# Kernel tuning notes

Measured on AMD Instinct MI355X. Metric: run time of the kernel, lower is better.

Reference implementation:

```python
import jax, jax.numpy as jnp
import numpy as np

CCA_W, INTRA_W, AUX_W, OS_W, RFS_W = 0.1, 0.05, 1.0, 1.0, 1.0


def cox_loss(risk, events, times):
    # Efron-tied Cox partial likelihood, vectorized over tie groups.
    order = jnp.argsort(-times)  # descending time
    r = risk[order]
    e = events[order]
    t = times[order]
    B = r.shape[0]
    max_r = jnp.max(r)
    exp_r = jnp.exp(r - max_r)
    cum = jnp.cumsum(exp_r)  # risk-set sums (descending time => cumsum)
    # contiguous tie groups (times sorted, ties adjacent)
    new_grp = jnp.concatenate([jnp.zeros(1, jnp.int32), (t[1:] != t[:-1]).astype(jnp.int32)])
    gid = jnp.cumsum(new_grp)
    rss = jax.ops.segment_max(cum, gid, num_segments=B)[gid]          # cum_exp_risk at last idx of group
    tes = jax.ops.segment_sum(exp_r * e, gid, num_segments=B)[gid]     # tied exp-risk sum
    d = jax.ops.segment_sum(e, gid, num_segments=B)[gid]               # tie count (events)
    # rank l of each event within its tie group (0..d-1)
    c = jnp.cumsum(e)
    start = jax.ops.segment_min(jnp.arange(B), gid, num_segments=B)[gid]
    before = c[start] - e[start]
    l = c - 1.0 - before
    d_safe = jnp.where(d > 0, d, 1.0)
    denom = rss - (l / d_safe) * tes
    contrib = e * (r - jnp.log(denom + 1e-12) - max_r)
    n_events = jnp.sum(e)
    return -jnp.sum(contrib) / (n_events + 1e-12)


def distance_correlation_loss(za, zb):
    def dist(x):
        xx = jnp.sum(x * x, axis=1, keepdims=True)
        d2 = xx + xx.T - 2.0 * (x @ x.T)
        return jnp.sqrt(jnp.maximum(d2, 1e-8))
    def dc(D):
        return D - D.mean(axis=1, keepdims=True) - D.mean(axis=0, keepdims=True) + D.mean()
    A = dc(dist(za))
    Bm = dc(dist(zb))
    dcov = jnp.mean(A * Bm)
    va = jnp.mean(A * A)
    vb = jnp.mean(Bm * Bm)
    return 1.0 - dcov / jnp.sqrt(jnp.maximum(va * vb, 1e-8))


def setup_inputs() -> dict:
    key = jax.random.key(0)
    ks = jax.random.split(key, 10)
    B, D = 8192, 256
    return {
        'risk_os': jax.random.normal(ks[0], (B,), jnp.float32),
        'risk_rfs': jax.random.normal(ks[1], (B,), jnp.float32),
        'z_ct': jax.random.normal(ks[2], (B, D), jnp.float32),
        'z_wsi': jax.random.normal(ks[3], (B, D), jnp.float32),
        'intra_wsi': jax.random.uniform(ks[4], (), jnp.float32),
        'intra_ct': jax.random.uniform(ks[5], (), jnp.float32),
        'evt_os': jax.random.randint(ks[6], (B,), 0, 2, jnp.int32),
        'tm_os': jax.random.randint(ks[7], (B,), 0, 1000, jnp.int32),
        'evt_rfs': jax.random.randint(ks[8], (B,), 0, 2, jnp.int32),
        'tm_rfs': jax.random.randint(ks[9], (B,), 0, 1000, jnp.int32),
    }


def reference(risk_os, risk_rfs, z_ct, z_wsi, intra_wsi, intra_ct,
              evt_os, tm_os, evt_rfs, tm_rfs):
    l_os = cox_loss(risk_os, evt_os.astype(jnp.float32), tm_os.astype(jnp.float32))
    l_rfs = cox_loss(risk_rfs, evt_rfs.astype(jnp.float32), tm_rfs.astype(jnp.float32))
    l_cca = distance_correlation_loss(z_ct, z_wsi)
    l_intra = intra_wsi + intra_ct
    total = OS_W * l_os + RFS_W * l_rfs + AUX_W * (CCA_W * l_cca + INTRA_W * l_intra)
    return total
```

## Files before the change

### kernel.cpp

```cpp
#include <hip/hip_runtime.h>
#include <hip/hip_bf16.h>
#include <math.h>

typedef __attribute__((ext_vector_type(4))) float f32x4;
typedef __attribute__((ext_vector_type(4))) int int4v;

#define NBINS 1000

__device__ __forceinline__ void gl16(const void* g, void* l) {
  __builtin_amdgcn_global_load_lds(
      (const __attribute__((address_space(1))) unsigned int*)g,
      (__attribute__((address_space(3))) unsigned int*)l, 16, 0, 0);
}

__device__ __forceinline__ float fp8mag(unsigned b) {
  const int e = (b >> 3) & 15;
  const int m = b & 7;
  return e ? ldexpf((float)(8 + m), e - 10) : ldexpf((float)m, -9);
}

__global__ __launch_bounds__(256)
void prep_kernel(const float* __restrict__ za, const float* __restrict__ zb,
                 float* __restrict__ na, float* __restrict__ nb,
                 unsigned char* __restrict__ zpa, unsigned char* __restrict__ zpb,
                 int B, int D)
{
  const int row = blockIdx.x * 4 + (threadIdx.x >> 6);
  const int lane = threadIdx.x & 63;
  const float* src; float* dst; unsigned char* bd; int r;
  if (row < B) { src = za; dst = na; bd = zpa; r = row; }
  else         { src = zb; dst = nb; bd = zpb; r = row - B; }
  const int pt = r >> 7;
  const int rr = r & 127;
  const int sw = (rr >> 1) & 3;
  const size_t tbase = (size_t)pt * 128 * D;
  float s = 0.f;
  for (int c = lane * 4; c < D; c += 256) {
    const f32x4 v = *(const f32x4*)&src[(size_t)r * D + c];
    unsigned u = (unsigned)__builtin_amdgcn_cvt_pk_fp8_f32(v[0], v[1], 0, false);
    u = (unsigned)__builtin_amdgcn_cvt_pk_fp8_f32(v[2], v[3], (int)u, true);
    const int sc = c >> 6;
    const int half = (c >> 5) & 1;
    const int kg = (c >> 3) & 3;
    const int rem = c & 7;
    const int slot = kg ^ sw;
    *(unsigned*)&bd[tbase + sc * 8192 + rr * 64 + slot * 16 + half * 8 + rem] = u;
    const float x0 = fp8mag(u & 255), x1 = fp8mag((u >> 8) & 255);
    const float x2 = fp8mag((u >> 16) & 255), x3 = fp8mag(u >> 24);
    s += x0 * x0 + x1 * x1 + x2 * x2 + x3 * x3;
  }
#pragma unroll
  for (int off = 32; off; off >>= 1) s += __shfl_xor(s, off);
  if (lane == 0) dst[r] = s;
}

__global__ __launch_bounds__(256, 2)
void dcor_kernel(const unsigned char* __restrict__ zpa,
                 const unsigned char* __restrict__ zpb,
                 const float* __restrict__ na, const float* __restrict__ nb,
                 float* __restrict__ Ra, float* __restrict__ Rb,
                 double* __restrict__ scalPart,
                 const float* __restrict__ r0, const int* __restrict__ e0, const int* __restrict__ t0,
                 const float* __restrict__ r1, const int* __restrict__ e1, const int* __restrict__ t1,
                 float* __restrict__ coxo,
                 int T, int nt, int B, int D)
{
  __shared__ __align__(16) union SU {
    unsigned char g[2][32768];
    struct { float sS[NBINS], sT[NBINS], sDc[NBINS], sc0[NBINS], sc1[NBINS], red[16], red3[48]; } c;
  } u;

  const int tid = threadIdx.x;
  const int bid = blockIdx.x;

  if (bid < 2) {
    const float* risk = bid ? r1 : r0;
    const int* evt = bid ? e1 : e0;
    const int* tm  = bid ? t1 : t0;
    const int NT = 256;

    float m = -3.0e38f;
    for (int i = tid; i < B; i += NT) m = fmaxf(m, risk[i]);
#pragma unroll
    for (int off = 32; off; off >>= 1) m = fmaxf(m, __shfl_xor(m, off));
    if ((tid & 63) == 0) u.c.red[tid >> 6] = m;
    __syncthreads();
    if (tid == 0) {
      float mm = u.c.red[0];
      for (int wv = 1; wv < 4; ++wv) mm = fmaxf(mm, u.c.red[wv]);
      u.c.red[0] = mm;
    }
    __syncthreads();
    const float maxr = u.c.red[0];

    for (int i = tid; i < NBINS; i += NT) { u.c.sS[i] = 0.f; u.c.sT[i] = 0.f; u.c.sDc[i] = 0.f; }
    __syncthreads();

    float sr = 0.f, nev = 0.f;
    for (int i = tid; i < B; i += NT) {
      const float r = risk[i];
      int t = tm[i];
      t = t < 0 ? 0 : (t >= NBINS ? NBINS - 1 : t);
      const float ex = expf(r - maxr);
      atomicAdd(&u.c.sS[t], ex);
      if (evt[i]) {
        atomicAdd(&u.c.sT[t], ex);
        atomicAdd(&u.c.sDc[t], 1.0f);
        sr += r; nev += 1.0f;
      }
    }
    __syncthreads();

    for (int i = tid; i < NBINS; i += NT) u.c.sc0[i] = u.c.sS[i];
    __syncthreads();
    float* pin = u.c.sc0; float* pout = u.c.sc1;
    for (int off = 1; off < NBINS; off <<= 1) {
      for (int i = tid; i < NBINS; i += NT) {
        float v = pin[i];
        if (i + off < NBINS) v += pin[i + off];
        pout[i] = v;
      }
      __syncthreads();
      float* tmp = pin; pin = pout; pout = tmp;
    }

    float ls = 0.f;
    for (int t = tid; t < NBINS; t += NT) {
      const float d = u.c.sDc[t];
      if (d > 0.f) {
        const float tes = u.c.sT[t];
        const float rs = pin[t];
        for (float l = 0.f; l < d - 0.5f; l += 1.f)
          ls += logf(rs - (l / d) * tes + 1e-12f);
      }
    }

    float v1 = sr, v2 = nev, v3 = ls;
#pragma unroll
    for (int off = 32; off; off >>= 1) {
      v1 += __shfl_xor(v1, off); v2 += __shfl_xor(v2, off); v3 += __shfl_xor(v3, off);
    }
    if ((tid & 63) == 0) { int wv = tid >> 6; u.c.red3[wv] = v1; u.c.red3[16 + wv] = v2; u.c.red3[32 + wv] = v3; }
    __syncthreads();
    if (tid == 0) {
      float SR = 0.f, NEV = 0.f, LS = 0.f;
      for (int wv = 0; wv < 4; ++wv) { SR += u.c.red3[wv]; NEV += u.c.red3[16 + wv]; LS += u.c.red3[32 + wv]; }
      coxo[bid] = -(SR - LS - NEV * maxr) / (NEV + 1e-12f);
    }
    return;
  }

  const int lane = tid & 63;
  const int w = tid >> 6;
  const int p = bid - 2;

  const int xcd = p & 7, pos = p >> 3;
  const int q = (xcd < 6 ? xcd * 64 : 384 + (xcd - 6) * 63) + pos;
  const int start = 4 * q + (q + 12) / 13;
  const int cnt = 4 + ((q % 13) == 0 ? 1 : 0);

  const double tn = (double)(2 * nt + 1);
  int ib0 = (int)((tn - sqrt(tn * tn - 8.0 * (double)start)) * 0.5);
  if (ib0 < 0) ib0 = 0;
  if (ib0 > nt - 1) ib0 = nt - 1;
  while (((ib0 + 1) * nt - ((ib0 + 1) * ib0) / 2) <= start) ++ib0;
  while ((ib0 * nt - (ib0 * (ib0 - 1)) / 2) > start) --ib0;
  const int jb0 = ib0 + (start - (ib0 * nt - (ib0 * (ib0 - 1)) / 2));

  const int gofs = w * 2048 + lane * 16;
  const int lofs = w * 2048;

  int sib = ib0, sjb = jb0;
  int cib = ib0, cjb = jb0;
  const unsigned char* gAi = zpa + (size_t)sib * 32768;
  const unsigned char* gAj = zpa + (size_t)sjb * 32768;
  const unsigned char* gBi = zpb + (size_t)sib * 32768;
  const unsigned char* gBj = zpb + (size_t)sjb * 32768;

#define STAGE(par_, sc_) do {                                        \
    const size_t co_ = (size_t)(sc_) * 8192 + gofs;                  \
    unsigned char* lb_ = &u.g[par_][lofs];                           \
    gl16(gAi + co_,        lb_);                                     \
    gl16(gAi + co_ + 1024, lb_ + 1024);                              \
    gl16(gAj + co_,        lb_ + 8192);                              \
    gl16(gAj + co_ + 1024, lb_ + 9216);                              \
    gl16(gBi + co_,        lb_ + 16384);                             \
    gl16(gBi + co_ + 1024, lb_ + 17408);                             \
    gl16(gBj + co_,        lb_ + 24576);                             \
    gl16(gBj + co_ + 1024, lb_ + 25600);                             \
  } while (0)

  const int wr = w >> 1, wc = w & 1;
  const int lrow = lane & 15;
  const int kg = lane >> 4;
  const int kgx = kg ^ ((lrow >> 1) & 3);
  const int abase = (wr * 64 + lrow) * 64 + kgx * 16;
  const int bbase = (wc * 64 + lrow) * 64 + kgx * 16;

  union I4L { int4v v; long l[2]; };

  const f32x4 Z4 = {0.f, 0.f, 0.f, 0.f};
  f32x4 accA[4][4], accB[4][4];
#pragma unroll
  for (int m = 0; m < 4; ++m)
#pragma unroll
    for (int n = 0; n < 4; ++n) { accA[m][n] = Z4; accB[m][n] = Z4; }

  const int S = cnt * 4;
  STAGE(0, 0);
  STAGE(1, 1);

  for (int s = 0; s < S; ++s) {
    const int k = s & 3;
    const int par = s & 1;

    if (s < S - 1) asm volatile("s_waitcnt vmcnt(8)" ::: "memory");
    else           asm volatile("s_waitcnt vmcnt(0)" ::: "memory");
    __builtin_amdgcn_sched_barrier(0);
    __builtin_amdgcn_s_barrier();
    __builtin_amdgcn_sched_barrier(0);

    {
      const unsigned char* lAi = &u.g[par][0];
      const unsigned char* lAj = &u.g[par][8192];
      I4L aA[4], bA[4];
#pragma unroll
      for (int m2 = 0; m2 < 4; ++m2) {
        aA[m2].v = *(const int4v*)&lAi[abase + m2 * 1024];
        bA[m2].v = *(const int4v*)&lAj[bbase + m2 * 1024];
      }
      __builtin_amdgcn_s_setprio(1);
#pragma unroll
      for (int m2 = 0; m2 < 4; ++m2)
#pragma unroll
        for (int n2 = 0; n2 < 4; ++n2) {
          accA[m2][n2] = __builtin_amdgcn_mfma_f32_16x16x32_fp8_fp8(aA[m2].l[0], bA[n2].l[0], accA[m2][n2], 0, 0, 0);
          accA[m2][n2] = __builtin_amdgcn_mfma_f32_16x16x32_fp8_fp8(aA[m2].l[1], bA[n2].l[1], accA[m2][n2], 0, 0, 0);
        }
      __builtin_amdgcn_s_setprio(0);
      const unsigned char* lBi = &u.g[par][16384];
      const unsigned char* lBj = &u.g[par][24576];
      I4L aB[4], bB[4];
#pragma unroll
      for (int m2 = 0; m2 < 4; ++m2) {
        aB[m2].v = *(const int4v*)&lBi[abase + m2 * 1024];
        bB[m2].v = *(const int4v*)&lBj[bbase + m2 * 1024];
      }
      __builtin_amdgcn_s_setprio(1);
#pragma unroll
      for (int m2 = 0; m2 < 4; ++m2)
#pragma unroll
        for (int n2 = 0; n2 < 4; ++n2) {
          accB[m2][n2] = __builtin_amdgcn_mfma_f32_16x16x32_fp8_fp8(aB[m2].l[0], bB[n2].l[0], accB[m2][n2], 0, 0, 0);
          accB[m2][n2] = __builtin_amdgcn_mfma_f32_16x16x32_fp8_fp8(aB[m2].l[1], bB[n2].l[1], accB[m2][n2], 0, 0, 0);
        }
      __builtin_amdgcn_s_setprio(0);
    }

    __builtin_amdgcn_sched_barrier(0);
    __builtin_amdgcn_s_barrier();
    __builtin_amdgcn_sched_barrier(0);

    if (s + 2 < S) {
      const int s2 = s + 2;
      if ((s2 & 3) == 0) {
        if (++sjb == nt) { ++sib; sjb = sib; }
        gAi = zpa + (size_t)sib * 32768;
        gAj = zpa + (size_t)sjb * 32768;
        gBi = zpb + (size_t)sib * 32768;
        gBj = zpb + (size_t)sjb * 32768;
      }
      STAGE(par, s2 & 3);
    }

    if (k == 3) {
      const bool offd = (cjb != cib);
      const float fac = offd ? 2.0f : 1.0f;
      float pab = 0.f, paa = 0.f, pbb = 0.f;
      float rsa[4][4], rsb[4][4];
      float csa[4] = {0.f, 0.f, 0.f, 0.f}, csb[4] = {0.f, 0.f, 0.f, 0.f};
#pragma unroll
      for (int m2 = 0; m2 < 4; ++m2)
#pragma unroll
        for (int r = 0; r < 4; ++r) { rsa[m2][r] = 0.f; rsb[m2][r] = 0.f; }

      const int gi0 = cib * 128 + wr * 64;
      const int gj0 = cjb * 128 + wc * 64;

#pragma unroll
      for (int m2 = 0; m2 < 4; ++m2) {
        const int gr = gi0 + m2 * 16 + kg * 4;
        const f32x4 nai = *(const f32x4*)&na[gr];
        const f32x4 nbi = *(const f32x4*)&nb[gr];
#pragma unroll
        for (int n2 = 0; n2 < 4; ++n2) {
          const int gc = gj0 + n2 * 16 + lrow;
          const float naj = na[gc];
          const float nbj = nb[gc];
          const f32x4 ga = accA[m2][n2];
          const f32x4 gb = accB[m2][n2];
#pragma unroll
          for (int r = 0; r < 4; ++r) {
            const float d2a = fmaxf(nai[r] + naj - 2.0f * ga[r], 1e-8f);
            const float d2b = fmaxf(nbi[r] + nbj - 2.0f * gb[r], 1e-8f);
            const float Da = __builtin_amdgcn_sqrtf(d2a);
            const float Db = __builtin_amdgcn_sqrtf(d2b);
            pab += Da * Db;
            paa += d2a;
            pbb += d2b;
            rsa[m2][r] += Da;
            rsb[m2][r] += Db;
            csa[n2] += Da;
            csb[n2] += Db;
          }
        }
      }

#pragma unroll
      for (int m2 = 0; m2 < 4; ++m2)
#pragma unroll
        for (int r = 0; r < 4; ++r) {
          float va = rsa[m2][r], vb = rsb[m2][r];
          va += __shfl_xor(va, 1); va += __shfl_xor(va, 2); va += __shfl_xor(va, 4); va += __shfl_xor(va, 8);
          vb += __shfl_xor(vb, 1); vb += __shfl_xor(vb, 2); vb += __shfl_xor(vb, 4); vb += __shfl_xor(vb, 8);
          if (lrow == 0) {
            const int gi = gi0 + m2 * 16 + kg * 4 + r;
            atomicAdd(&Ra[gi], va);
            atomicAdd(&Rb[gi], vb);
          }
        }

      if (offd) {
#pragma unroll
        for (int n2 = 0; n2 < 4; ++n2) {
          float va = csa[n2], vb = csb[n2];
          va += __shfl_xor(va, 16); va += __shfl_xor(va, 32);
          vb += __shfl_xor(vb, 16); vb += __shfl_xor(vb, 32);
          if (kg == 0) {
            const int gj = gj0 + n2 * 16 + lrow;
            atomicAdd(&Ra[gj], va);
            atomicAdd(&Rb[gj], vb);
          }
        }
      }

      float q1 = fac * pab, q2 = fac * paa, q3 = fac * pbb;
#pragma unroll
      for (int off = 32; off; off >>= 1) {
        q1 += __shfl_xor(q1, off); q2 += __shfl_xor(q2, off); q3 += __shfl_xor(q3, off);
      }
      if (lane == 0) {
        const int ctile = start + (s >> 2);
        double* sp = scalPart + (size_t)ctile * 12 + w * 3;
        sp[0] = (double)q1; sp[1] = (double)q2; sp[2] = (double)q3;
      }

      if (++cjb == nt) { ++cib; cjb = cib; }
#pragma unroll
      for (int m2 = 0; m2 < 4; ++m2)
#pragma unroll
        for (int n2 = 0; n2 < 4; ++n2) { accA[m2][n2] = Z4; accB[m2][n2] = Z4; }
    }
  }
#undef STAGE
}

__global__ __launch_bounds__(256)
void finalize_kernel(const float* __restrict__ Ra, const float* __restrict__ Rb,
                     const double* __restrict__ scalPart, int T,
                     const float* __restrict__ coxo,
                     const float* __restrict__ iw, const float* __restrict__ ic,
                     float* __restrict__ out, int B)
{
  const int tid = threadIdx.x;
  double v[8];
#pragma unroll
  for (int k = 0; k < 8; ++k) v[k] = 0.0;
  for (int i = tid; i < B; i += 256) {
    const double a = Ra[i], b = Rb[i];
    v[0] += a; v[1] += b; v[2] += a * b; v[3] += a * a; v[4] += b * b;
  }
  for (int i = tid; i < T; i += 256) {
    const double* sp = scalPart + (size_t)i * 12;
    v[5] += sp[0] + sp[3] + sp[6] + sp[9];
    v[6] += sp[1] + sp[4] + sp[7] + sp[10];
    v[7] += sp[2] + sp[5] + sp[8] + sp[11];
  }
#pragma unroll
  for (int k = 0; k < 8; ++k)
#pragma unroll
    for (int off = 32; off; off >>= 1) v[k] += __shfl_xor(v[k], off);
  __shared__ double sred[32];
  const int w = tid >> 6;
  if ((tid & 63) == 0) {
#pragma unroll
    for (int k = 0; k < 8; ++k) sred[k * 4 + w] = v[k];
  }
  __syncthreads();
  if (tid == 0) {
    double r[8];
#pragma unroll
    for (int k = 0; k < 8; ++k) r[k] = sred[k * 4] + sred[k * 4 + 1] + sred[k * 4 + 2] + sred[k * 4 + 3];
    const double ta = r[0], tb = r[1], sab = r[2], saa = r[3], sbb = r[4];
    const double Pab = r[5], Paa = r[6], Pbb = r[7];
    const double n = (double)B;
    const double Sab = Pab - (2.0 / n) * sab + ta * tb / (n * n);
    const double Saa = Paa - (2.0 / n) * saa + ta * ta / (n * n);
    const double Sbb = Pbb - (2.0 / n) * sbb + tb * tb / (n * n);
    const double dcov = Sab / (n * n);
    const double va = Saa / (n * n);
    const double vb = Sbb / (n * n);
    const double l_cca = 1.0 - dcov / sqrt(fmax(va * vb, 1e-8));
    const double total = (double)coxo[0] + (double)coxo[1]
                       + (0.1 * l_cca + 0.05 * ((double)iw[0] + (double)ic[0]));
    out[0] = (float)total;
  }
}

extern "C" void kernel_launch(void* const* d_in, const int* in_sizes, int n_in,
                              void* d_out, int out_size, void* d_ws, size_t ws_size,
                              hipStream_t stream)
{
  (void)n_in; (void)out_size; (void)ws_size;
  const float* risk_os   = (const float*)d_in[0];
  const float* risk_rfs  = (const float*)d_in[1];
  const float* z_ct      = (const float*)d_in[2];
  const float* z_wsi     = (const float*)d_in[3];
  const float* intra_wsi = (const float*)d_in[4];
  const float* intra_ct  = (const float*)d_in[5];
  const int* evt_os  = (const int*)d_in[6];
  const int* tm_os   = (const int*)d_in[7];
  const int* evt_rfs = (const int*)d_in[8];
  const int* tm_rfs  = (const int*)d_in[9];

  const int B = in_sizes[0];
  const int D = in_sizes[2] / B;
  const int nt = B / 128;
  const int T = nt * (nt + 1) / 2;

  float* ws = (float*)d_ws;
  float* Ra = ws;
  float* Rb = ws + B;
  float* coxo = ws + 2 * B;
  float* na  = ws + 2 * B + 16;
  float* nbv = ws + 3 * B + 16;
  double* scalPart = (double*)(ws + 4 * B + 16);
  unsigned char* zpa = (unsigned char*)(ws + 4 * B + 16 + 24 * T);
  unsigned char* zpb = zpa + (size_t)B * D;

  (void)hipMemsetAsync(d_ws, 0, (size_t)(2 * B) * sizeof(float), stream);

  prep_kernel<<<(2 * B) / 4, 256, 0, stream>>>(z_ct, z_wsi, na, nbv, zpa, zpb, B, D);
  dcor_kernel<<<512, 256, 0, stream>>>(zpa, zpb, na, nbv, Ra, Rb, scalPart,
                                       risk_os, evt_os, tm_os, risk_rfs, evt_rfs, tm_rfs,
                                       coxo, T, nt, B, D);
  finalize_kernel<<<1, 256, 0, stream>>>(Ra, Rb, scalPart, T, coxo, intra_wsi, intra_ct, (float*)d_out, B);
}
```

Measured before the change: 103.7 us.

## Halve K-stage size, raise occupancy to 3 blocks/CU, rebalance tile distribution

Changes the fp8 packed layout to 32-wide K chunks, so each pipeline stage stages half as much data (16KB double buffer instead of 32KB). This allows launch bounds of 3 blocks per CU and 768 blocks with 3 or 2 tiles each instead of 4-5. Per-tile scalar partials are accumulated in registers and written once per wave, which shrinks the finalize reduction. The cost is more barriers and stages per tile, with single MFMA per fragment pair per stage, and fewer registers available per thread.

```diff
diff --git a/kernel.cpp b/kernel.cpp
--- a/kernel.cpp
+++ b/kernel.cpp
@@ -3,7 +3,6 @@
 #include <math.h>
 
 typedef __attribute__((ext_vector_type(4))) float f32x4;
-typedef __attribute__((ext_vector_type(4))) int int4v;
 
 #define NBINS 1000
 
@@ -30,21 +29,19 @@
   const float* src; float* dst; unsigned char* bd; int r;
   if (row < B) { src = za; dst = na; bd = zpa; r = row; }
   else         { src = zb; dst = nb; bd = zpb; r = row - B; }
-  const int pt = r >> 7;
   const int rr = r & 127;
-  const int sw = (rr >> 1) & 3;
-  const size_t tbase = (size_t)pt * 128 * D;
+  const int sw = (rr >> 2) & 3;
+  const size_t tbase = (size_t)(r >> 7) * 128 * D;
   float s = 0.f;
   for (int c = lane * 4; c < D; c += 256) {
     const f32x4 v = *(const f32x4*)&src[(size_t)r * D + c];
     unsigned u = (unsigned)__builtin_amdgcn_cvt_pk_fp8_f32(v[0], v[1], 0, false);
     u = (unsigned)__builtin_amdgcn_cvt_pk_fp8_f32(v[2], v[3], (int)u, true);
-    const int sc = c >> 6;
-    const int half = (c >> 5) & 1;
+    const int kc = c >> 5;
     const int kg = (c >> 3) & 3;
     const int rem = c & 7;
-    const int slot = kg ^ sw;
-    *(unsigned*)&bd[tbase + sc * 8192 + rr * 64 + slot * 16 + half * 8 + rem] = u;
+    const int phys = kg ^ sw;
+    *(unsigned*)&bd[tbase + kc * 4096 + rr * 32 + phys * 8 + rem] = u;
     const float x0 = fp8mag(u & 255), x1 = fp8mag((u >> 8) & 255);
     const float x2 = fp8mag((u >> 16) & 255), x3 = fp8mag(u >> 24);
     s += x0 * x0 + x1 * x1 + x2 * x2 + x3 * x3;
@@ -54,7 +51,7 @@
   if (lane == 0) dst[r] = s;
 }
 
-__global__ __launch_bounds__(256, 2)
+__global__ __launch_bounds__(256, 3)
 void dcor_kernel(const unsigned char* __restrict__ zpa,
                  const unsigned char* __restrict__ zpb,
                  const float* __restrict__ na, const float* __restrict__ nb,
@@ -63,10 +60,10 @@
                  const float* __restrict__ r0, const int* __restrict__ e0, const int* __restrict__ t0,
                  const float* __restrict__ r1, const int* __restrict__ e1, const int* __restrict__ t1,
                  float* __restrict__ coxo,
-                 int T, int nt, int B, int D)
+                 int nt, int B, int D)
 {
   __shared__ __align__(16) union SU {
-    unsigned char g[2][32768];
+    unsigned char g[2][16384];
     struct { float sS[NBINS], sT[NBINS], sDc[NBINS], sc0[NBINS], sc1[NBINS], red[16], red3[48]; } c;
   } u;
 
@@ -155,9 +152,9 @@
   const int p = bid - 2;
 
   const int xcd = p & 7, pos = p >> 3;
-  const int q = (xcd < 6 ? xcd * 64 : 384 + (xcd - 6) * 63) + pos;
-  const int start = 4 * q + (q + 12) / 13;
-  const int cnt = 4 + ((q % 13) == 0 ? 1 : 0);
+  const int q = (xcd < 6 ? xcd * 96 : 576 + (xcd - 6) * 95) + pos;
+  const int start = (q < 548) ? 3 * q : 1644 + 2 * (q - 548);
+  const int cnt = (q < 548) ? 3 : 2;
 
   const double tn = (double)(2 * nt + 1);
   int ib0 = (int)((tn - sqrt(tn * tn - 8.0 * (double)start)) * 0.5);
@@ -167,8 +164,8 @@
   while ((ib0 * nt - (ib0 * (ib0 - 1)) / 2) > start) --ib0;
   const int jb0 = ib0 + (start - (ib0 * nt - (ib0 * (ib0 - 1)) / 2));
 
-  const int gofs = w * 2048 + lane * 16;
-  const int lofs = w * 2048;
+  const int gofs = w * 1024 + lane * 16;
+  const int lofs = w * 1024;
 
   int sib = ib0, sjb = jb0;
   int cib = ib0, cjb = jb0;
@@ -177,44 +174,40 @@
   const unsigned char* gBi = zpb + (size_t)sib * 32768;
   const unsigned char* gBj = zpb + (size_t)sjb * 32768;
 
-#define STAGE(par_, sc_) do {                                        \
-    const size_t co_ = (size_t)(sc_) * 8192 + gofs;                  \
+#define STAGE(par_, kc_) do {                                        \
+    const size_t co_ = (size_t)(kc_) * 4096 + gofs;                  \
     unsigned char* lb_ = &u.g[par_][lofs];                           \
-    gl16(gAi + co_,        lb_);                                     \
-    gl16(gAi + co_ + 1024, lb_ + 1024);                              \
-    gl16(gAj + co_,        lb_ + 8192);                              \
-    gl16(gAj + co_ + 1024, lb_ + 9216);                              \
-    gl16(gBi + co_,        lb_ + 16384);                             \
-    gl16(gBi + co_ + 1024, lb_ + 17408);                             \
-    gl16(gBj + co_,        lb_ + 24576);                             \
-    gl16(gBj + co_ + 1024, lb_ + 25600);                             \
+    gl16(gAi + co_, lb_);                                            \
+    gl16(gAj + co_, lb_ + 4096);                                     \
+    gl16(gBi + co_, lb_ + 8192);                                     \
+    gl16(gBj + co_, lb_ + 12288);                                    \
   } while (0)
 
   const int wr = w >> 1, wc = w & 1;
   const int lrow = lane & 15;
   const int kg = lane >> 4;
-  const int kgx = kg ^ ((lrow >> 1) & 3);
-  const int abase = (wr * 64 + lrow) * 64 + kgx * 16;
-  const int bbase = (wc * 64 + lrow) * 64 + kgx * 16;
-
-  union I4L { int4v v; long l[2]; };
+  const int kswz = kg ^ ((lrow >> 2) & 3);
+  const int abase = (wr * 64 + lrow) * 32 + kswz * 8;
+  const int bbase = (wc * 64 + lrow) * 32 + kswz * 8;
 
   const f32x4 Z4 = {0.f, 0.f, 0.f, 0.f};
   f32x4 accA[4][4], accB[4][4];
 #pragma unroll
-  for (int m = 0; m < 4; ++m)
-#pragma unroll
-    for (int n = 0; n < 4; ++n) { accA[m][n] = Z4; accB[m][n] = Z4; }
-
-  const int S = cnt * 4;
+  for (int m2 = 0; m2 < 4; ++m2)
+#pragma unroll
+    for (int n2 = 0; n2 < 4; ++n2) { accA[m2][n2] = Z4; accB[m2][n2] = Z4; }
+
+  double dp0 = 0.0, dp1 = 0.0, dp2 = 0.0;
+
+  const int S = cnt * 8;
   STAGE(0, 0);
   STAGE(1, 1);
 
   for (int s = 0; s < S; ++s) {
-    const int k = s & 3;
+    const int k = s & 7;
     const int par = s & 1;
 
-    if (s < S - 1) asm volatile("s_waitcnt vmcnt(8)" ::: "memory");
+    if (s < S - 1) asm volatile("s_waitcnt vmcnt(4)" ::: "memory");
     else           asm volatile("s_waitcnt vmcnt(0)" ::: "memory");
     __builtin_amdgcn_sched_barrier(0);
     __builtin_amdgcn_s_barrier();
@@ -222,38 +215,32 @@
 
     {
       const unsigned char* lAi = &u.g[par][0];
-      const unsigned char* lAj = &u.g[par][8192];
-      I4L aA[4], bA[4];
-#pragma unroll
-      for (int m2 = 0; m2 < 4; ++m2) {
-        aA[m2].v = *(const int4v*)&lAi[abase + m2 * 1024];
-        bA[m2].v = *(const int4v*)&lAj[bbase + m2 * 1024];
-      }
+      const unsigned char* lAj = &u.g[par][4096];
+      long aA[4], bA[4];
+#pragma unroll
+      for (int m2 = 0; m2 < 4; ++m2) aA[m2] = *(const long*)&lAi[abase + m2 * 512];
+#pragma unroll
+      for (int n2 = 0; n2 < 4; ++n2) bA[n2] = *(const long*)&lAj[bbase + n2 * 512];
       __builtin_amdgcn_s_setprio(1);
 #pragma unroll
       for (int m2 = 0; m2 < 4; ++m2)
 #pragma unroll
-        for (int n2 = 0; n2 < 4; ++n2) {
-          accA[m2][n2] = __builtin_amdgcn_mfma_f32_16x16x32_fp8_fp8(aA[m2].l[0], bA[n2].l[0], accA[m2][n2], 0, 0, 0);
-          accA[m2][n2] = __builtin_amdgcn_mfma_f32_16x16x32_fp8_fp8(aA[m2].l[1], bA[n2].l[1], accA[m2][n2], 0, 0, 0);
-        }
+        for (int n2 = 0; n2 < 4; ++n2)
+          accA[m2][n2] = __builtin_amdgcn_mfma_f32_16x16x32_fp8_fp8(aA[m2], bA[n2], accA[m2][n2], 0, 0, 0);
       __builtin_amdgcn_s_setprio(0);
-      const unsigned char* lBi = &u.g[par][16384];
-      const unsigned char* lBj = &u.g[par][24576];
-      I4L aB[4], bB[4];
-#pragma unroll
-      for (int m2 = 0; m2 < 4; ++m2) {
-        aB[m2].v = *(const int4v*)&lBi[abase + m2 * 1024];
-        bB[m2].v = *(const int4v*)&lBj[bbase + m2 * 1024];
-      }
+      const unsigned char* lBi = &u.g[par][8192];
+      const unsigned char* lBj = &u.g[par][12288];
+      long aB[4], bB[4];
+#pragma unroll
+      for (int m2 = 0; m2 < 4; ++m2) aB[m2] = *(const long*)&lBi[abase + m2 * 512];
+#pragma unroll
+      for (int n2 = 0; n2 < 4; ++n2) bB[n2] = *(const long*)&lBj[bbase + n2 * 512];
       __builtin_amdgcn_s_setprio(1);
 #pragma unroll
       for (int m2 = 0; m2 < 4; ++m2)
 #pragma unroll
-        for (int n2 = 0; n2 < 4; ++n2) {
-          accB[m2][n2] = __builtin_amdgcn_mfma_f32_16x16x32_fp8_fp8(aB[m2].l[0], bB[n2].l[0], accB[m2][n2], 0, 0, 0);
-          accB[m2][n2] = __builtin_amdgcn_mfma_f32_16x16x32_fp8_fp8(aB[m2].l[1], bB[n2].l[1], accB[m2][n2], 0, 0, 0);
-        }
+        for (int n2 = 0; n2 < 4; ++n2)
+          accB[m2][n2] = __builtin_amdgcn_mfma_f32_16x16x32_fp8_fp8(aB[m2], bB[n2], accB[m2][n2], 0, 0, 0);
       __builtin_amdgcn_s_setprio(0);
     }
 
@@ -263,17 +250,17 @@
 
     if (s + 2 < S) {
       const int s2 = s + 2;
-      if ((s2 & 3) == 0) {
+      if ((s2 & 7) == 0) {
         if (++sjb == nt) { ++sib; sjb = sib; }
         gAi = zpa + (size_t)sib * 32768;
         gAj = zpa + (size_t)sjb * 32768;
         gBi = zpb + (size_t)sib * 32768;
         gBj = zpb + (size_t)sjb * 32768;
       }
-      STAGE(par, s2 & 3);
-    }
-
-    if (k == 3) {
+      STAGE(par, s2 & 7);
+    }
+
+    if (k == 7) {
       const bool offd = (cjb != cib);
       const float fac = offd ? 2.0f : 1.0f;
       float pab = 0.f, paa = 0.f, pbb = 0.f;
@@ -349,11 +336,7 @@
       for (int off = 32; off; off >>= 1) {
         q1 += __shfl_xor(q1, off); q2 += __shfl_xor(q2, off); q3 += __shfl_xor(q3, off);
       }
-      if (lane == 0) {
-        const int ctile = start + (s >> 2);
-        double* sp = scalPart + (size_t)ctile * 12 + w * 3;
-        sp[0] = (double)q1; sp[1] = (double)q2; sp[2] = (double)q3;
-      }
+      dp0 += (double)q1; dp1 += (double)q2; dp2 += (double)q3;
 
       if (++cjb == nt) { ++cib; cjb = cib; }
 #pragma unroll
@@ -363,11 +346,16 @@
     }
   }
 #undef STAGE
+
+  if (lane == 0) {
+    double* sp = scalPart + (size_t)(p * 4 + w) * 3;
+    sp[0] = dp0; sp[1] = dp1; sp[2] = dp2;
+  }
 }
 
 __global__ __launch_bounds__(256)
 void finalize_kernel(const float* __restrict__ Ra, const float* __restrict__ Rb,
-                     const double* __restrict__ scalPart, int T,
+                     const double* __restrict__ scalPart, int NS,
                      const float* __restrict__ coxo,
                      const float* __restrict__ iw, const float* __restrict__ ic,
                      float* __restrict__ out, int B)
@@ -380,11 +368,9 @@
     const double a = Ra[i], b = Rb[i];
     v[0] += a; v[1] += b; v[2] += a * b; v[3] += a * a; v[4] += b * b;
   }
-  for (int i = tid; i < T; i += 256) {
-    const double* sp = scalPart + (size_t)i * 12;
-    v[5] += sp[0] + sp[3] + sp[6] + sp[9];
-    v[6] += sp[1] + sp[4] + sp[7] + sp[10];
-    v[7] += sp[2] + sp[5] + sp[8] + sp[11];
+  for (int i = tid; i < NS; i += 256) {
+    const double* sp = scalPart + (size_t)i * 3;
+    v[5] += sp[0]; v[6] += sp[1]; v[7] += sp[2];
   }
 #pragma unroll
   for (int k = 0; k < 8; ++k)
@@ -436,7 +422,7 @@
   const int B = in_sizes[0];
   const int D = in_sizes[2] / B;
   const int nt = B / 128;
-  const int T = nt * (nt + 1) / 2;
+  const int NS = 766 * 4;
 
   float* ws = (float*)d_ws;
   float* Ra = ws;
@@ -445,14 +431,14 @@
   float* na  = ws + 2 * B + 16;
   float* nbv = ws + 3 * B + 16;
   double* scalPart = (double*)(ws + 4 * B + 16);
-  unsigned char* zpa = (unsigned char*)(ws + 4 * B + 16 + 24 * T);
+  unsigned char* zpa = (unsigned char*)(ws + 4 * B + 16 + 6 * NS + 8);
   unsigned char* zpb = zpa + (size_t)B * D;
 
   (void)hipMemsetAsync(d_ws, 0, (size_t)(2 * B) * sizeof(float), stream);
 
   prep_kernel<<<(2 * B) / 4, 256, 0, stream>>>(z_ct, z_wsi, na, nbv, zpa, zpb, B, D);
-  dcor_kernel<<<512, 256, 0, stream>>>(zpa, zpb, na, nbv, Ra, Rb, scalPart,
+  dcor_kernel<<<768, 256, 0, stream>>>(zpa, zpb, na, nbv, Ra, Rb, scalPart,
                                        risk_os, evt_os, tm_os, risk_rfs, evt_rfs, tm_rfs,
-                                       coxo, T, nt, B, D);
-  finalize_kernel<<<1, 256, 0, stream>>>(Ra, Rb, scalPart, T, coxo, intra_wsi, intra_ct, (float*)d_out, B);
-}
+                                       coxo, nt, B, D);
+  finalize_kernel<<<1, 256, 0, stream>>>(Ra, Rb, scalPart, NS, coxo, intra_wsi, intra_ct, (float*)d_out, B);
+}
```

New measurement: 159.8 us. +54.1%, slower.
